# Optimization experiments

Hardware: AMD Instinct MI355X
Metric: run time of the kernel (lower is better)

Reference implementation:

```python
import jax, jax.numpy as jnp
import numpy as np

TEMPERATURE = 0.07


def setup_inputs() -> dict:
    key = jax.random.key(0)
    k1, k2 = jax.random.split(key)
    B, V, D = 4096, 5, 512
    img = jax.random.normal(k1, (B, D), dtype=jnp.float32)
    txt = jax.random.normal(k2, (B, V, D), dtype=jnp.float32)
    # module assumes pre-normalized features
    img = img / jnp.linalg.norm(img, axis=-1, keepdims=True)
    txt = txt / jnp.linalg.norm(txt, axis=-1, keepdims=True)
    return {"image_features": img, "text_features_all": txt}


def reference(image_features, text_features_all):
    B, V, D = text_features_all.shape
    text_flat = text_features_all.reshape(B * V, D)          # (BV, D)
    logits = (image_features @ text_flat.T) / TEMPERATURE    # (B, BV)

    # i2t: per image-row, soft targets = 1/V on its V positive texts
    row_lse = jax.nn.logsumexp(logits, axis=1)               # (B,)
    pos_logits = logits.reshape(B, B, V)[jnp.arange(B), jnp.arange(B)]  # (B, V)
    loss_i2t = jnp.mean(row_lse - jnp.mean(pos_logits, axis=1))

    # t2i: per text-column, cross-entropy over B images, target = col // V
    col_lse = jax.nn.logsumexp(logits, axis=0)               # (BV,)
    img_idx = jnp.arange(B * V) // V
    pos_col = logits[img_idx, jnp.arange(B * V)]             # (BV,)
    loss_t2i = jnp.mean(col_lse - pos_col)

    return (loss_i2t + loss_t2i) * 0.5
```

## Files before the change

kernel.cpp:

```cpp
#include <hip/hip_runtime.h>
#include <stdint.h>

#define B_  4096
#define V_  5
#define D_  512
#define NN_ (B_ * V_)
#define NBLK_ 5120

#define C_EXP 20.609929155556620f
#define M_SHIFT (1.0f / 0.07f)
#define SCALE1 0x7f7f7f7f

typedef float floatx4 __attribute__((ext_vector_type(4)));
typedef int   intx4   __attribute__((ext_vector_type(4)));
typedef int   intx8   __attribute__((ext_vector_type(8)));

__device__ __forceinline__ void load_lds16(const void* g, void* l) {
  __builtin_amdgcn_global_load_lds(
      (const __attribute__((address_space(1))) unsigned int*)g,
      (__attribute__((address_space(3))) unsigned int*)l,
      16, 0, 0);
}

__global__ void cvt_kernel(const float* __restrict__ img, const float* __restrict__ txt,
                           uint8_t* __restrict__ out8, float* __restrict__ acc) {
  const int t = blockIdx.x * 256 + threadIdx.x;
  if (t < B_ + NN_) acc[t] = 0.0f;
  const float4* src; int g;
  if (t < (B_ * D_) / 16) { src = (const float4*)img; g = t; }
  else                    { src = (const float4*)txt; g = t - (B_ * D_) / 16; }
  float4 a = src[4 * g + 0], b = src[4 * g + 1];
  float4 c = src[4 * g + 2], d = src[4 * g + 3];
  int w0 = __builtin_amdgcn_cvt_pk_fp8_f32(a.x, a.y, 0, 0);
  w0     = __builtin_amdgcn_cvt_pk_fp8_f32(a.z, a.w, w0, 1);
  int w1 = __builtin_amdgcn_cvt_pk_fp8_f32(b.x, b.y, 0, 0);
  w1     = __builtin_amdgcn_cvt_pk_fp8_f32(b.z, b.w, w1, 1);
  int w2 = __builtin_amdgcn_cvt_pk_fp8_f32(c.x, c.y, 0, 0);
  w2     = __builtin_amdgcn_cvt_pk_fp8_f32(c.z, c.w, w2, 1);
  int w3 = __builtin_amdgcn_cvt_pk_fp8_f32(d.x, d.y, 0, 0);
  w3     = __builtin_amdgcn_cvt_pk_fp8_f32(d.z, d.w, w3, 1);
  ((int4*)out8)[t] = make_int4(w0, w1, w2, w3);
}

__global__ __launch_bounds__(256, 3)
void gemm_kernel(const uint8_t* __restrict__ Ah, const uint8_t* __restrict__ Bh,
                 float* __restrict__ row_sum, float* __restrict__ col_sum,
                 float* __restrict__ posPart) {
  __shared__ __align__(16) uint8_t As[2 * 128 * 64];
  __shared__ __align__(16) uint8_t Bs[2 * 128 * 64];
  const int tid  = threadIdx.x;
  const int lane = tid & 63;
  const int w    = tid >> 6;
  const int wm   = w >> 1, wn = w & 1;
  const int m0   = blockIdx.x * 128;
  const int n0   = blockIdx.y * 128;

  floatx4 acc[4][4] = {};

  const int sc = ((lane & 3) ^ ((lane >> 3) & 3)) * 16;
  const uint8_t* gA = Ah + (size_t)(m0 + w * 32 + (lane >> 2)) * D_ + sc;
  const uint8_t* gB = Bh + (size_t)(n0 + w * 32 + (lane >> 2)) * D_ + sc;
  const int lofs = (w * 32) * 64;

  const int fr  = lane & 15;
  const int swz = (fr >> 1) & 3;
  const int qb  = (lane >> 5) & 1;
  const int qh  = (lane >> 4) & 1;
  const int c0  = ((qh * 2 + 0) ^ swz) * 16;
  const int c1  = ((qh * 2 + 1) ^ swz) * 16;
  const int bufo = qb * 8192;

  load_lds16(gA,                &As[lofs]);
  load_lds16(gA + 16 * D_,      &As[lofs + 16 * 64]);
  load_lds16(gB,                &Bs[lofs]);
  load_lds16(gB + 16 * D_,      &Bs[lofs + 16 * 64]);
  load_lds16(gA + 64,           &As[8192 + lofs]);
  load_lds16(gA + 64 + 16 * D_, &As[8192 + lofs + 16 * 64]);
  load_lds16(gB + 64,           &Bs[8192 + lofs]);
  load_lds16(gB + 64 + 16 * D_, &Bs[8192 + lofs + 16 * 64]);

  for (int ss = 0; ss < 4; ++ss) {
    __syncthreads();

    intx8 af[4], bf[4];
#pragma unroll
    for (int f = 0; f < 4; ++f) {
      const uint8_t* Ar = As + bufo + (wm * 64 + f * 16 + fr) * 64;
      const uint8_t* Br = Bs + bufo + (wn * 64 + f * 16 + fr) * 64;
      intx4 alo = *(const intx4*)(Ar + c0);
      intx4 ahi = *(const intx4*)(Ar + c1);
      intx4 blo = *(const intx4*)(Br + c0);
      intx4 bhi = *(const intx4*)(Br + c1);
      af[f] = __builtin_shufflevector(alo, ahi, 0, 1, 2, 3, 4, 5, 6, 7);
      bf[f] = __builtin_shufflevector(blo, bhi, 0, 1, 2, 3, 4, 5, 6, 7);
    }

    __syncthreads();

    if (ss < 3) {
      const int kg = (2 * ss + 2) * 64;
      load_lds16(gA + kg,                &As[lofs]);
      load_lds16(gA + kg + 16 * D_,      &As[lofs + 16 * 64]);
      load_lds16(gB + kg,                &Bs[lofs]);
      load_lds16(gB + kg + 16 * D_,      &Bs[lofs + 16 * 64]);
      load_lds16(gA + kg + 64,           &As[8192 + lofs]);
      load_lds16(gA + kg + 64 + 16 * D_, &As[8192 + lofs + 16 * 64]);
      load_lds16(gB + kg + 64,           &Bs[8192 + lofs]);
      load_lds16(gB + kg + 64 + 16 * D_, &Bs[8192 + lofs + 16 * 64]);
    }

#pragma unroll
    for (int mf = 0; mf < 4; ++mf)
#pragma unroll
      for (int nf = 0; nf < 4; ++nf)
        acc[mf][nf] = __builtin_amdgcn_mfma_scale_f32_16x16x128_f8f6f4(
            af[mf], bf[nf], acc[mf][nf],
            0, 0,
            0, SCALE1,
            0, SCALE1);
  }

  {
    float ps = 0.0f;
    const int iLo = n0 / 5, iHi = (n0 + 127) / 5;
    if (iHi >= m0 && iLo < m0 + 128) {
      const int rbase = m0 + wm * 64 + ((lane >> 4) << 2);
#pragma unroll
      for (int nf = 0; nf < 4; ++nf) {
        const int ci = (n0 + wn * 64 + nf * 16 + (lane & 15)) / 5;
#pragma unroll
        for (int mf = 0; mf < 4; ++mf)
#pragma unroll
          for (int r = 0; r < 4; ++r)
            if (rbase + mf * 16 + r == ci) ps += acc[mf][nf][r];
      }
    }
    for (int o = 32; o; o >>= 1) ps += __shfl_xor(ps, o);
    __shared__ float pls[4];
    if (lane == 0) pls[w] = ps;
    __syncthreads();
    if (tid == 0)
      posPart[blockIdx.y * 32 + blockIdx.x] = pls[0] + pls[1] + pls[2] + pls[3];
  }

#pragma unroll
  for (int mf = 0; mf < 4; ++mf)
#pragma unroll
    for (int nf = 0; nf < 4; ++nf)
#pragma unroll
      for (int r = 0; r < 4; ++r)
        acc[mf][nf][r] = exp2f(acc[mf][nf][r] * C_EXP - C_EXP);

  float cs[4];
#pragma unroll
  for (int nf = 0; nf < 4; ++nf) {
    float s = 0.0f;
#pragma unroll
    for (int mf = 0; mf < 4; ++mf)
      s += acc[mf][nf][0] + acc[mf][nf][1] + acc[mf][nf][2] + acc[mf][nf][3];
    s += __shfl_xor(s, 16);
    s += __shfl_xor(s, 32);
    cs[nf] = s;
  }
  {
    int g = lane >> 4;
    float v = (g == 0) ? cs[0] : (g == 1) ? cs[1] : (g == 2) ? cs[2] : cs[3];
    atomicAdd(&col_sum[n0 + wn * 64 + (g << 4) + (lane & 15)], v);
  }

#pragma unroll
  for (int mf = 0; mf < 4; ++mf) {
    floatx4 t = acc[mf][0] + acc[mf][1] + acc[mf][2] + acc[mf][3];
#pragma unroll
    for (int r = 0; r < 4; ++r) {
      float s = t[r];
      s += __shfl_xor(s, 1); s += __shfl_xor(s, 2);
      s += __shfl_xor(s, 4); s += __shfl_xor(s, 8);
      t[r] = s;
    }
    if ((lane & 15) < 4) {
      int q = lane & 3;
      float v = (q == 0) ? t[0] : (q == 1) ? t[1] : (q == 2) ? t[2] : t[3];
      atomicAdd(&row_sum[m0 + wm * 64 + mf * 16 + ((lane >> 4) << 2) + q], v);
    }
  }
}

__global__ void finish_kernel(const float* __restrict__ acc, const float* __restrict__ posPart,
                              float* __restrict__ out) {
  int tid = threadIdx.x;
  float sA = 0.0f, sB = 0.0f, sP = 0.0f;
  for (int i = tid; i < B_;    i += 1024) sA += logf(acc[i]);
  for (int i = tid; i < NN_;   i += 1024) sB += logf(acc[B_ + i]);
  for (int i = tid; i < NBLK_; i += 1024) sP += posPart[i];
  float s = sA * (1.0f / B_) + sB * (1.0f / NN_)
          - sP * (2.0f * M_SHIFT / (float)NN_);
  for (int o = 32; o; o >>= 1) s += __shfl_xor(s, o);
  __shared__ float ls[16];
  int lane = tid & 63, w = tid >> 6;
  if (lane == 0) ls[w] = s;
  __syncthreads();
  if (tid == 0) {
    float tot = 0.0f;
#pragma unroll
    for (int i = 0; i < 16; ++i) tot += ls[i];
    out[0] = M_SHIFT + 0.5f * tot;
  }
}

extern "C" void kernel_launch(void* const* d_in, const int* in_sizes, int n_in,
                              void* d_out, int out_size, void* d_ws, size_t ws_size,
                              hipStream_t stream) {
  const float* img = (const float*)d_in[0];
  const float* txt = (const float*)d_in[1];

  const size_t fp8Bytes = (size_t)(B_ * D_ + NN_ * D_);
  const size_t needBytes = fp8Bytes + (size_t)(B_ + NN_ + NBLK_) * 4;
  if (ws_size < needBytes) return;

  uint8_t* Ah  = (uint8_t*)d_ws;
  uint8_t* Bh  = Ah + (size_t)B_ * D_;
  float* acc   = (float*)((char*)d_ws + fp8Bytes);
  float* row_s = acc;
  float* col_s = acc + B_;
  float* posP  = acc + B_ + NN_;

  cvt_kernel   <<<3072, 256, 0, stream>>>(img, txt, Ah, acc);
  gemm_kernel  <<<dim3(32, 160), 256, 0, stream>>>(Ah, Bh, row_s, col_s, posP);
  finish_kernel<<<1, 1024, 0, stream>>>(acc, posP, (float*)d_out);
}
```

Baseline: 159.4 us.

## Double-buffer LDS tiles so global loads of next k-stage overlap fragment reads

Doubles the LDS buffers for the A and B tiles. The loads for the next k-stage are now issued into the alternate buffer right after the barrier, and the second barrier per iteration is removed. This lets global-to-LDS transfers overlap the fragment reads and the MFMA work, and it halves the number of barriers. In exchange LDS use doubles to 64KB per block and launch bounds drop from 3 to 2 blocks per CU, which reduces occupancy.

```diff
diff --git a/kernel.cpp b/kernel.cpp
--- a/kernel.cpp
+++ b/kernel.cpp
@@ -42,12 +42,12 @@
   ((int4*)out8)[t] = make_int4(w0, w1, w2, w3);
 }
 
-__global__ __launch_bounds__(256, 3)
+__global__ __launch_bounds__(256, 2)
 void gemm_kernel(const uint8_t* __restrict__ Ah, const uint8_t* __restrict__ Bh,
                  float* __restrict__ row_sum, float* __restrict__ col_sum,
                  float* __restrict__ posPart) {
-  __shared__ __align__(16) uint8_t As[2 * 128 * 64];
-  __shared__ __align__(16) uint8_t Bs[2 * 128 * 64];
+  __shared__ __align__(16) uint8_t As[2][2 * 128 * 64];
+  __shared__ __align__(16) uint8_t Bs[2][2 * 128 * 64];
   const int tid  = threadIdx.x;
   const int lane = tid & 63;
   const int w    = tid >> 6;
@@ -70,23 +70,31 @@
   const int c1  = ((qh * 2 + 1) ^ swz) * 16;
   const int bufo = qb * 8192;
 
-  load_lds16(gA,                &As[lofs]);
-  load_lds16(gA + 16 * D_,      &As[lofs + 16 * 64]);
-  load_lds16(gB,                &Bs[lofs]);
-  load_lds16(gB + 16 * D_,      &Bs[lofs + 16 * 64]);
-  load_lds16(gA + 64,           &As[8192 + lofs]);
-  load_lds16(gA + 64 + 16 * D_, &As[8192 + lofs + 16 * 64]);
-  load_lds16(gB + 64,           &Bs[8192 + lofs]);
-  load_lds16(gB + 64 + 16 * D_, &Bs[8192 + lofs + 16 * 64]);
+  #define STAGE(s, A, B) do {                                      \
+    const int kg = (s) * 128;                                      \
+    load_lds16(gA + kg,                (A) + lofs);                \
+    load_lds16(gA + kg + 16 * D_,      (A) + lofs + 16 * 64);      \
+    load_lds16(gB + kg,                (B) + lofs);                \
+    load_lds16(gB + kg + 16 * D_,      (B) + lofs + 16 * 64);      \
+    load_lds16(gA + kg + 64,           (A) + 8192 + lofs);         \
+    load_lds16(gA + kg + 64 + 16 * D_, (A) + 8192 + lofs + 16 * 64); \
+    load_lds16(gB + kg + 64,           (B) + 8192 + lofs);         \
+    load_lds16(gB + kg + 64 + 16 * D_, (B) + 8192 + lofs + 16 * 64); \
+  } while (0)
+
+  STAGE(0, As[0], Bs[0]);
 
   for (int ss = 0; ss < 4; ++ss) {
+    const int p = ss & 1;
     __syncthreads();
 
+    if (ss < 3) STAGE(ss + 1, As[1 - p], Bs[1 - p]);
+
     intx8 af[4], bf[4];
 #pragma unroll
     for (int f = 0; f < 4; ++f) {
-      const uint8_t* Ar = As + bufo + (wm * 64 + f * 16 + fr) * 64;
-      const uint8_t* Br = Bs + bufo + (wn * 64 + f * 16 + fr) * 64;
+      const uint8_t* Ar = As[p] + bufo + (wm * 64 + f * 16 + fr) * 64;
+      const uint8_t* Br = Bs[p] + bufo + (wn * 64 + f * 16 + fr) * 64;
       intx4 alo = *(const intx4*)(Ar + c0);
       intx4 ahi = *(const intx4*)(Ar + c1);
       intx4 blo = *(const intx4*)(Br + c0);
@@ -95,20 +103,6 @@
       bf[f] = __builtin_shufflevector(blo, bhi, 0, 1, 2, 3, 4, 5, 6, 7);
     }
 
-    __syncthreads();
-
-    if (ss < 3) {
-      const int kg = (2 * ss + 2) * 64;
-      load_lds16(gA + kg,                &As[lofs]);
-      load_lds16(gA + kg + 16 * D_,      &As[lofs + 16 * 64]);
-      load_lds16(gB + kg,                &Bs[lofs]);
-      load_lds16(gB + kg + 16 * D_,      &Bs[lofs + 16 * 64]);
-      load_lds16(gA + kg + 64,           &As[8192 + lofs]);
-      load_lds16(gA + kg + 64 + 16 * D_, &As[8192 + lofs + 16 * 64]);
-      load_lds16(gB + kg + 64,           &Bs[8192 + lofs]);
-      load_lds16(gB + kg + 64 + 16 * D_, &Bs[8192 + lofs + 16 * 64]);
-    }
-
 #pragma unroll
     for (int mf = 0; mf < 4; ++mf)
 #pragma unroll
@@ -119,6 +113,7 @@
             0, SCALE1,
             0, SCALE1);
   }
+  #undef STAGE
 
   {
     float ps = 0.0f;
```

New measurement: 176.9 us. 1.11x slower.
